# Kernel tuning notes

Measured on AMD Instinct MI355X. Metric: run time of the kernel, lower is better.

## Reference

```python
import jax, jax.numpy as jnp
import numpy as np

D_MODEL = 1024
N_HEADS = 16
D_HEAD = D_MODEL // N_HEADS
B, T = 2, 2048


def setup_inputs() -> dict:
    key = jax.random.key(0)
    k1, k2, k3, k4, k5 = jax.random.split(key, 5)
    s = 1.0 / np.sqrt(D_MODEL)
    return {
        "x": jax.random.normal(k1, (B, T, D_MODEL), dtype=jnp.float32),
        "w_attn": jax.random.normal(k2, (D_MODEL, 3 * D_MODEL), dtype=jnp.float32) * s,
        "b_attn": jax.random.normal(k3, (3 * D_MODEL,), dtype=jnp.float32) * 0.01,
        "w_proj": jax.random.normal(k4, (D_MODEL, D_MODEL), dtype=jnp.float32) * s,
        "b_proj": jax.random.normal(k5, (D_MODEL,), dtype=jnp.float32) * 0.01,
    }


def reference(x, w_attn, b_attn, w_proj, b_proj):
    # x: [B, T, D]. Math is exact causal softmax attention; the torch module's
    # tiled online-softmax loop computes the identical result.
    Bn, Tn, Dn = x.shape
    qkv = x @ w_attn + b_attn                       # [B, T, 3D]
    q, k, v = jnp.split(qkv, 3, axis=-1)

    def heads(t):
        return t.reshape(Bn, Tn, N_HEADS, D_HEAD).transpose(0, 2, 1, 3)  # [B,H,T,d]

    q, k, v = heads(q), heads(k), heads(v)
    scale = D_HEAD ** -0.5
    scores = jnp.einsum("bhqd,bhkd->bhqk", q, k) * scale  # [B,H,T,T]
    causal = jnp.tril(jnp.ones((Tn, Tn), dtype=bool))
    scores = jnp.where(causal, scores, -jnp.inf)
    p = jax.nn.softmax(scores, axis=-1)
    o = jnp.einsum("bhqk,bhkd->bhqd", p, v)
    o = o.transpose(0, 2, 1, 3).reshape(Bn, Tn, Dn)
    return o @ w_proj + b_proj
```

## Files before the change

kernel.cpp:

```cpp
#include <hip/hip_runtime.h>


#define B_   2
#define T_   2048
#define D_   1024
#define H_   16
#define DH_  64
#define M_   (B_ * T_)
#define N1_  (3 * D_)
#define QSCALE (0.125f * 1.44269504088896340736f)

typedef __bf16 bf16x8 __attribute__((ext_vector_type(8)));
typedef __bf16 bf16x4 __attribute__((ext_vector_type(4)));
typedef float  f32x4  __attribute__((ext_vector_type(4)));

#define MFMA16(a, b, c) __builtin_amdgcn_mfma_f32_16x16x32_bf16((a), (b), (c), 0, 0, 0)

#define GLOAD16(gp, lp)                                                        \
    __builtin_amdgcn_global_load_lds(                                          \
        (const __attribute__((address_space(1))) void*)(gp),                   \
        (__attribute__((address_space(3))) void*)(lp), 16, 0, 0)

#define DRAIN_ALL() __asm__ volatile("s_waitcnt vmcnt(0) lgkmcnt(0)" ::: "memory")


__global__ void f32_to_bf16_kernel(const float* __restrict__ in,
                                   __bf16* __restrict__ out, int n) {
    int i = (blockIdx.x * blockDim.x + threadIdx.x) * 4;
    if (i + 3 < n) {
        float4 f = *(const float4*)(in + i);
        bf16x4 o;
        o[0] = (__bf16)f.x; o[1] = (__bf16)f.y; o[2] = (__bf16)f.z; o[3] = (__bf16)f.w;
        *(bf16x4*)(out + i) = o;
    }
}

__global__ void transpose_bf16_kernel(const float* __restrict__ in,
                                      __bf16* __restrict__ out, int R, int C) {
    __shared__ float tile[32][33];
    int tx = threadIdx.x;
    int ty = threadIdx.y;
    int c0 = blockIdx.x * 32;
    int r0 = blockIdx.y * 32;
#pragma unroll
    for (int i = 0; i < 4; i++)
        tile[ty + i * 8][tx] = in[(size_t)(r0 + ty + i * 8) * C + c0 + tx];
    __syncthreads();
#pragma unroll
    for (int i = 0; i < 4; i++)
        out[(size_t)(c0 + ty + i * 8) * R + r0 + tx] = (__bf16)tile[tx][ty + i * 8];
}


template <int EPI, int TM>
__global__ __launch_bounds__(256) void gemm_bt_kernel(
    const __bf16* __restrict__ A, const __bf16* __restrict__ Bt,
    const float* __restrict__ bias, float* __restrict__ Cout,
    __bf16* __restrict__ Q, __bf16* __restrict__ Kb, __bf16* __restrict__ Vt,
    int M, int N, int K) {
    constexpr int MI  = TM / 32;
    constexpr int WM  = MI * 16;
    constexpr int ACH = TM / 64;
    __shared__ __bf16 As[2][TM * 32];
    __shared__ __bf16 Bs[2][128 * 32];

    const int tid  = threadIdx.x;
    const int lane = tid & 63;
    const int wave = tid >> 6;
    const int lo   = lane & 15;
    const int qd   = lane >> 4;
    const int wm   = (wave >> 1) * WM;
    const int wn   = (wave & 1) * 64;
    const int m0   = blockIdx.y * TM;
    const int n0   = blockIdx.x * 128;

    const __bf16* gA[ACH];
    const __bf16* gB[2];
#pragma unroll
    for (int c = 0; c < ACH; c++) {
        int g = tid + 256 * c;
        gA[c] = A + (size_t)(m0 + (g >> 2)) * K + (g & 3) * 8;
    }
#pragma unroll
    for (int c = 0; c < 2; c++) {
        int g = tid + 256 * c;
        gB[c] = Bt + (size_t)(n0 + (g >> 2)) * K + (g & 3) * 8;
    }

    f32x4 acc[MI][4] = {};
    const int nk = K >> 5;

#pragma unroll
    for (int c = 0; c < ACH; c++)
        GLOAD16(gA[c], (__bf16*)As[0] + (tid + 256 * c) * 8);
#pragma unroll
    for (int c = 0; c < 2; c++)
        GLOAD16(gB[c], (__bf16*)Bs[0] + (tid + 256 * c) * 8);
    DRAIN_ALL();
    __syncthreads();

    for (int kt = 0; kt < nk; kt++) {
        const int cur = kt & 1;
        if (kt + 1 < nk) {
            const int k0n = (kt + 1) << 5;
#pragma unroll
            for (int c = 0; c < ACH; c++)
                GLOAD16(gA[c] + k0n, (__bf16*)As[1 - cur] + (tid + 256 * c) * 8);
#pragma unroll
            for (int c = 0; c < 2; c++)
                GLOAD16(gB[c] + k0n, (__bf16*)Bs[1 - cur] + (tid + 256 * c) * 8);
        }
        bf16x8 af[MI], bfr[4];
#pragma unroll
        for (int i = 0; i < MI; i++)
            af[i] = *(const bf16x8*)(As[cur] + (wm + i * 16 + lo) * 32 + qd * 8);
#pragma unroll
        for (int j = 0; j < 4; j++)
            bfr[j] = *(const bf16x8*)(Bs[cur] + (wn + j * 16 + lo) * 32 + qd * 8);
#pragma unroll
        for (int i = 0; i < MI; i++)
#pragma unroll
            for (int j = 0; j < 4; j++)
                acc[i][j] = MFMA16(af[i], bfr[j], acc[i][j]);
        DRAIN_ALL();
        __syncthreads();
    }

#pragma unroll
    for (int i = 0; i < MI; i++) {
#pragma unroll
        for (int j = 0; j < 4; j++) {
#pragma unroll
            for (int r = 0; r < 4; r++) {
                int gm = m0 + wm + i * 16 + qd * 4 + r;
                int gn = n0 + wn + j * 16 + lo;
                float v = acc[i][j][r] + bias[gn];
                if (EPI == 1) {
                    Cout[(size_t)gm * N + gn] = v;
                } else {
                    int which = gn >> 10;
                    int bh = ((gm >> 11) << 4) + ((gn >> 6) & 15);
                    int dd = gn & 63;
                    int t  = gm & (T_ - 1);
                    if (which == 0)
                        Q[((size_t)bh * T_ + t) * DH_ + dd] = (__bf16)(v * QSCALE);
                    else if (which == 1)
                        Kb[((size_t)bh * T_ + t) * DH_ + dd] = (__bf16)v;
                    else
                        Vt[((size_t)bh * DH_ + dd) * T_ + t] = (__bf16)v;
                }
            }
        }
    }
}


__global__ __launch_bounds__(256) void attn_kernel(
    const __bf16* __restrict__ Q,
    const __bf16* __restrict__ Kb,
    const __bf16* __restrict__ Vt,
    __bf16* __restrict__ O) {
    __shared__ __bf16 Ks[2][64 * 64];
    __shared__ __bf16 Vs[2][64 * 64];
    __shared__ __bf16 Ps[4][16][72];

    const int tid  = threadIdx.x;
    const int wave = tid >> 6;
    const int lane = tid & 63;
    const int lo   = lane & 15;
    const int qd   = lane >> 4;

    const int g0  = wave * 128 + lane;
    const int g1  = g0 + 64;
    const int r0s = g0 >> 3, c0s = (g0 & 7) ^ (r0s & 7);
    const int r1s = g1 >> 3, c1s = (g1 & 7) ^ (r1s & 7);
    const int so0 = wave * 1024;
    const int so1 = wave * 1024 + 512;

    bf16x8 ones;
#pragma unroll
    for (int i = 0; i < 8; i++) ones[i] = (__bf16)1.0f;

    const int kblk   = blockIdx.x;
    const int nitems = (kblk >= 512) ? 2 : 1;

    for (int it = 0; it < nitems; it++) {
        const int item = (it == 0) ? kblk : (1535 - kblk);
        const int x    = 31 - (item >> 5);
        const int bh   = item & 31;
        const int b    = bh >> 4;
        const int h    = bh & 15;
        const int q0   = x * 64 + wave * 16;

        const __bf16* Qh = Q + (size_t)bh * T_ * DH_;
        const __bf16* Kh = Kb + (size_t)bh * T_ * DH_;
        const __bf16* Vh = Vt + (size_t)bh * DH_ * T_;

        bf16x8 qa0 = *(const bf16x8*)(Qh + (size_t)(q0 + lo) * DH_ + qd * 8);
        bf16x8 qa1 = *(const bf16x8*)(Qh + (size_t)(q0 + lo) * DH_ + 32 + qd * 8);

        f32x4 oacc[4] = {};
        float m = -1e30f;
        float lrow[4] = {0.0f, 0.0f, 0.0f, 0.0f};
        const int qrow  = q0 + qd * 4;
        const int ntile = x + 1;

        GLOAD16(Kh + (size_t)r0s * DH_ + c0s * 8, Ks[0] + so0);
        GLOAD16(Kh + (size_t)r1s * DH_ + c1s * 8, Ks[0] + so1);
        GLOAD16(Vh + (size_t)r0s * T_ + c0s * 8, Vs[0] + so0);
        GLOAD16(Vh + (size_t)r1s * T_ + c1s * 8, Vs[0] + so1);
        DRAIN_ALL();
        __syncthreads();

        for (int t = 0; t < ntile; t++) {
            const int j0  = t << 6;
            const int cur = t & 1;
            if (t + 1 < ntile) {
                const int j0n = j0 + 64;
                GLOAD16(Kh + (size_t)(j0n + r0s) * DH_ + c0s * 8, Ks[1 - cur] + so0);
                GLOAD16(Kh + (size_t)(j0n + r1s) * DH_ + c1s * 8, Ks[1 - cur] + so1);
                GLOAD16(Vh + (size_t)r0s * T_ + j0n + c0s * 8, Vs[1 - cur] + so0);
                GLOAD16(Vh + (size_t)r1s * T_ + j0n + c1s * 8, Vs[1 - cur] + so1);
            }

            f32x4 s[4] = {};
#pragma unroll
            for (int g = 0; g < 4; g++) {
                const int row = g * 16 + lo;
                const __bf16* kr = Ks[cur] + row * 64;
                bf16x8 kb0 = *(const bf16x8*)(kr + ((qd ^ (row & 7)) << 3));
                bf16x8 kb1 = *(const bf16x8*)(kr + (((4 + qd) ^ (row & 7)) << 3));
                s[g] = MFMA16(qa0, kb0, s[g]);
                s[g] = MFMA16(qa1, kb1, s[g]);
            }

            if (j0 + 63 > q0) {
#pragma unroll
                for (int g = 0; g < 4; g++) {
                    const int col = j0 + g * 16 + lo;
#pragma unroll
                    for (int r = 0; r < 4; r++)
                        s[g][r] = (col <= qrow + r) ? s[g][r] : -1e30f;
                }
            }

            float lm = s[0][0];
#pragma unroll
            for (int g = 0; g < 4; g++)
#pragma unroll
                for (int r = 0; r < 4; r++) lm = fmaxf(lm, s[g][r]);
#pragma unroll
            for (int off = 1; off < 64; off <<= 1)
                lm = fmaxf(lm, __shfl_xor(lm, off));
            const float mnew = fmaxf(m, lm);
            if (mnew > m) {
                const float alpha = __builtin_amdgcn_exp2f(m - mnew);
#pragma unroll
                for (int r = 0; r < 4; r++) lrow[r] *= alpha;
#pragma unroll
                for (int c = 0; c < 4; c++)
#pragma unroll
                    for (int r = 0; r < 4; r++) oacc[c][r] *= alpha;
                m = mnew;
            }

#pragma unroll
            for (int g = 0; g < 4; g++)
#pragma unroll
                for (int r = 0; r < 4; r++)
                    Ps[wave][qd * 4 + r][g * 16 + lo] =
                        (__bf16)__builtin_amdgcn_exp2f(s[g][r] - m);
            __asm__ volatile("s_waitcnt lgkmcnt(0)" ::: "memory");
            bf16x8 pa0 = *(const bf16x8*)(&Ps[wave][lo][qd * 8]);
            bf16x8 pa1 = *(const bf16x8*)(&Ps[wave][lo][32 + qd * 8]);

            f32x4 ps = {};
            ps = MFMA16(pa0, ones, ps);
            ps = MFMA16(pa1, ones, ps);
#pragma unroll
            for (int c = 0; c < 4; c++) {
                const int row = c * 16 + lo;
                const __bf16* vr = Vs[cur] + row * 64;
                bf16x8 vb0 = *(const bf16x8*)(vr + ((qd ^ (row & 7)) << 3));
                bf16x8 vb1 = *(const bf16x8*)(vr + (((4 + qd) ^ (row & 7)) << 3));
                oacc[c] = MFMA16(pa0, vb0, oacc[c]);
                oacc[c] = MFMA16(pa1, vb1, oacc[c]);
            }
#pragma unroll
            for (int r = 0; r < 4; r++) lrow[r] += ps[r];

            DRAIN_ALL();
            __syncthreads();
        }

        float inv[4];
#pragma unroll
        for (int r = 0; r < 4; r++) inv[r] = 1.0f / lrow[r];
#pragma unroll
        for (int c = 0; c < 4; c++) {
#pragma unroll
            for (int r = 0; r < 4; r++) {
                float val = oacc[c][r] * inv[r];
                size_t idx = ((size_t)b * T_ + (qrow + r)) * D_ + h * DH_ + c * 16 + lo;
                O[idx] = (__bf16)val;
            }
        }
    }
}


extern "C" void kernel_launch(void* const* d_in, const int* in_sizes, int n_in,
                              void* d_out, int out_size, void* d_ws, size_t ws_size,
                              hipStream_t stream) {
    const float* x      = (const float*)d_in[0];
    const float* w_attn = (const float*)d_in[1];
    const float* b_attn = (const float*)d_in[2];
    const float* w_proj = (const float*)d_in[3];
    const float* b_proj = (const float*)d_in[4];
    float* out = (float*)d_out;

    const size_t MB = (size_t)1 << 20;
    if (ws_size < 48 * MB) return;

    char* ws = (char*)d_ws;
    __bf16* xb     = (__bf16*)(ws);
    __bf16* wattnT = (__bf16*)(ws + 8 * MB);
    __bf16* wprojT = (__bf16*)(ws + 14 * MB);
    __bf16* Qb     = (__bf16*)(ws + 16 * MB);
    __bf16* Kb     = (__bf16*)(ws + 24 * MB);
    __bf16* Vt     = (__bf16*)(ws + 32 * MB);
    __bf16* Ob     = (__bf16*)(ws + 40 * MB);

    f32_to_bf16_kernel<<<(M_ * D_) / 1024, 256, 0, stream>>>(x, xb, M_ * D_);
    transpose_bf16_kernel<<<dim3(N1_ / 32, D_ / 32), dim3(32, 8), 0, stream>>>(
        w_attn, wattnT, D_, N1_);
    transpose_bf16_kernel<<<dim3(D_ / 32, D_ / 32), dim3(32, 8), 0, stream>>>(
        w_proj, wprojT, D_, D_);
    gemm_bt_kernel<0, 128><<<dim3(N1_ / 128, M_ / 128), 256, 0, stream>>>(
        xb, wattnT, b_attn, nullptr, Qb, Kb, Vt, M_, N1_, D_);
    attn_kernel<<<dim3(768), 256, 0, stream>>>(Qb, Kb, Vt, Ob);
    gemm_bt_kernel<1, 64><<<dim3(D_ / 128, M_ / 64), 256, 0, stream>>>(
        Ob, wprojT, b_proj, out, nullptr, nullptr, nullptr, M_, D_, D_);
}
```

Measured before the change: 197.5 us.

## Software-pipeline attention loop by deferring PV MFMAs to next iteration

Restructures the flash-attention inner loop so the P·V matrix multiplies and row-sum for tile t-1 run at the start of iteration t, overlapping with the QK^T MFMAs for tile t. V fragments and the P operands are held in registers across iterations, with a peeled prologue for tile 0 and an epilogue for the last tile. The running max is updated one tile late, so probabilities are exponentiated against a stale max and rescaled afterwards. This shortens the dependency chain on each tile but adds register pressure and a risk of larger exponent values before rescaling.

```diff
diff --git a/kernel.cpp b/kernel.cpp
--- a/kernel.cpp
+++ b/kernel.cpp
@@ -200,8 +200,10 @@
         bf16x8 qa1 = *(const bf16x8*)(Qh + (size_t)(q0 + lo) * DH_ + 32 + qd * 8);
 
         f32x4 oacc[4] = {};
-        float m = -1e30f;
         float lrow[4] = {0.0f, 0.0f, 0.0f, 0.0f};
+        float m, lmprev;
+        bf16x8 pa0, pa1;
+        bf16x8 vb[8];
         const int qrow  = q0 + qd * 4;
         const int ntile = x + 1;
 
@@ -212,7 +214,63 @@
         DRAIN_ALL();
         __syncthreads();
 
-        for (int t = 0; t < ntile; t++) {
+        {
+            if (ntile > 1) {
+                GLOAD16(Kh + (size_t)(64 + r0s) * DH_ + c0s * 8, Ks[1] + so0);
+                GLOAD16(Kh + (size_t)(64 + r1s) * DH_ + c1s * 8, Ks[1] + so1);
+                GLOAD16(Vh + (size_t)r0s * T_ + 64 + c0s * 8, Vs[1] + so0);
+                GLOAD16(Vh + (size_t)r1s * T_ + 64 + c1s * 8, Vs[1] + so1);
+            }
+            f32x4 s[4] = {};
+#pragma unroll
+            for (int g = 0; g < 4; g++) {
+                const int row = g * 16 + lo;
+                const __bf16* kr = Ks[0] + row * 64;
+                bf16x8 kb0 = *(const bf16x8*)(kr + ((qd ^ (row & 7)) << 3));
+                bf16x8 kb1 = *(const bf16x8*)(kr + (((4 + qd) ^ (row & 7)) << 3));
+                s[g] = MFMA16(qa0, kb0, s[g]);
+                s[g] = MFMA16(qa1, kb1, s[g]);
+            }
+            if (63 > q0) {
+#pragma unroll
+                for (int g = 0; g < 4; g++) {
+                    const int col = g * 16 + lo;
+#pragma unroll
+                    for (int r = 0; r < 4; r++)
+                        s[g][r] = (col <= qrow + r) ? s[g][r] : -1e30f;
+                }
+            }
+            float lm = s[0][0];
+#pragma unroll
+            for (int g = 0; g < 4; g++)
+#pragma unroll
+                for (int r = 0; r < 4; r++) lm = fmaxf(lm, s[g][r]);
+#pragma unroll
+            for (int off = 1; off < 64; off <<= 1)
+                lm = fmaxf(lm, __shfl_xor(lm, off));
+            m = lm;
+            lmprev = lm;
+#pragma unroll
+            for (int g = 0; g < 4; g++)
+#pragma unroll
+                for (int r = 0; r < 4; r++)
+                    Ps[wave][qd * 4 + r][g * 16 + lo] =
+                        (__bf16)__builtin_amdgcn_exp2f(s[g][r] - m);
+            __asm__ volatile("s_waitcnt lgkmcnt(0)" ::: "memory");
+            pa0 = *(const bf16x8*)(&Ps[wave][lo][qd * 8]);
+            pa1 = *(const bf16x8*)(&Ps[wave][lo][32 + qd * 8]);
+#pragma unroll
+            for (int c = 0; c < 4; c++) {
+                const int row = c * 16 + lo;
+                const __bf16* vr = Vs[0] + row * 64;
+                vb[c * 2]     = *(const bf16x8*)(vr + ((qd ^ (row & 7)) << 3));
+                vb[c * 2 + 1] = *(const bf16x8*)(vr + (((4 + qd) ^ (row & 7)) << 3));
+            }
+            DRAIN_ALL();
+            __syncthreads();
+        }
+
+        for (int t = 1; t < ntile; t++) {
             const int j0  = t << 6;
             const int cur = t & 1;
             if (t + 1 < ntile) {
@@ -223,6 +281,17 @@
                 GLOAD16(Vh + (size_t)r1s * T_ + j0n + c1s * 8, Vs[1 - cur] + so1);
             }
 
+            f32x4 ps = {};
+            ps = MFMA16(pa0, ones, ps);
+            ps = MFMA16(pa1, ones, ps);
+#pragma unroll
+            for (int c = 0; c < 4; c++) {
+                oacc[c] = MFMA16(pa0, vb[c * 2], oacc[c]);
+                oacc[c] = MFMA16(pa1, vb[c * 2 + 1], oacc[c]);
+            }
+#pragma unroll
+            for (int r = 0; r < 4; r++) lrow[r] += ps[r];
+
             f32x4 s[4] = {};
 #pragma unroll
             for (int g = 0; g < 4; g++) {
@@ -233,7 +302,6 @@
                 s[g] = MFMA16(qa0, kb0, s[g]);
                 s[g] = MFMA16(qa1, kb1, s[g]);
             }
-
             if (j0 + 63 > q0) {
 #pragma unroll
                 for (int g = 0; g < 4; g++) {
@@ -244,6 +312,20 @@
                 }
             }
 
+            {
+                const float mnew = fmaxf(m, lmprev);
+                if (mnew > m) {
+                    const float alpha = __builtin_amdgcn_exp2f(m - mnew);
+#pragma unroll
+                    for (int r = 0; r < 4; r++) lrow[r] *= alpha;
+#pragma unroll
+                    for (int c = 0; c < 4; c++)
+#pragma unroll
+                        for (int r = 0; r < 4; r++) oacc[c][r] *= alpha;
+                    m = mnew;
+                }
+            }
+
             float lm = s[0][0];
 #pragma unroll
             for (int g = 0; g < 4; g++)
@@ -252,17 +334,7 @@
 #pragma unroll
             for (int off = 1; off < 64; off <<= 1)
                 lm = fmaxf(lm, __shfl_xor(lm, off));
-            const float mnew = fmaxf(m, lm);
-            if (mnew > m) {
-                const float alpha = __builtin_amdgcn_exp2f(m - mnew);
-#pragma unroll
-                for (int r = 0; r < 4; r++) lrow[r] *= alpha;
-#pragma unroll
-                for (int c = 0; c < 4; c++)
-#pragma unroll
-                    for (int r = 0; r < 4; r++) oacc[c][r] *= alpha;
-                m = mnew;
-            }
+            lmprev = lm;
 
 #pragma unroll
             for (int g = 0; g < 4; g++)
@@ -271,28 +343,33 @@
                     Ps[wave][qd * 4 + r][g * 16 + lo] =
                         (__bf16)__builtin_amdgcn_exp2f(s[g][r] - m);
             __asm__ volatile("s_waitcnt lgkmcnt(0)" ::: "memory");
-            bf16x8 pa0 = *(const bf16x8*)(&Ps[wave][lo][qd * 8]);
-            bf16x8 pa1 = *(const bf16x8*)(&Ps[wave][lo][32 + qd * 8]);
-
+            pa0 = *(const bf16x8*)(&Ps[wave][lo][qd * 8]);
+            pa1 = *(const bf16x8*)(&Ps[wave][lo][32 + qd * 8]);
+
+#pragma unroll
+            for (int c = 0; c < 4; c++) {
+                const int row = c * 16 + lo;
+                const __bf16* vr = Vs[cur] + row * 64;
+                vb[c * 2]     = *(const bf16x8*)(vr + ((qd ^ (row & 7)) << 3));
+                vb[c * 2 + 1] = *(const bf16x8*)(vr + (((4 + qd) ^ (row & 7)) << 3));
+            }
+
+            DRAIN_ALL();
+            __syncthreads();
+        }
+
+        {
             f32x4 ps = {};
             ps = MFMA16(pa0, ones, ps);
             ps = MFMA16(pa1, ones, ps);
 #pragma unroll
             for (int c = 0; c < 4; c++) {
-                const int row = c * 16 + lo;
-                const __bf16* vr = Vs[cur] + row * 64;
-                bf16x8 vb0 = *(const bf16x8*)(vr + ((qd ^ (row & 7)) << 3));
-                bf16x8 vb1 = *(const bf16x8*)(vr + (((4 + qd) ^ (row & 7)) << 3));
-                oacc[c] = MFMA16(pa0, vb0, oacc[c]);
-                oacc[c] = MFMA16(pa1, vb1, oacc[c]);
+                oacc[c] = MFMA16(pa0, vb[c * 2], oacc[c]);
+                oacc[c] = MFMA16(pa1, vb[c * 2 + 1], oacc[c]);
             }
 #pragma unroll
             for (int r = 0; r < 4; r++) lrow[r] += ps[r];
-
-            DRAIN_ALL();
-            __syncthreads();
-        }
-
+        }
         float inv[4];
 #pragma unroll
         for (int r = 0; r < 4; r++) inv[r] = 1.0f / lrow[r];
```

New measurement: 206.2 us. +4.4%, slower.
